# Performance work log

Hardware: AMD Instinct MI355X
Metric: run time of the kernel (lower is better)

Reference implementation:

```python
import jax, jax.numpy as jnp
import numpy as np

S, L = 4096, 12
VOCAB, CHARS, TAGS = 100000, 128, 64
CE, CH, WE, H = 64, 128, 256, 512


def setup_inputs() -> dict:
    key = jax.random.key(0)
    ks = jax.random.split(key, 16)
    n = lambda k, shp, s=0.05: (jax.random.normal(k, shp, jnp.float32) * s)
    return {
        "w_seq": jax.random.randint(ks[0], (S,), 0, VOCAB),
        "c_seq": jax.random.randint(ks[1], (S, L), 0, CHARS),
        "char_emb": n(ks[2], (CHARS, CE), 1.0),
        "word_emb": n(ks[3], (VOCAB, WE), 1.0),
        "c_hx0": jnp.zeros((CH,), jnp.float32),
        "c_cx0": jnp.zeros((CH,), jnp.float32),
        "hx0": jnp.zeros((H,), jnp.float32),
        "cx0": jnp.zeros((H,), jnp.float32),
        "Wih1": n(ks[4], (4 * CH, CE)),
        "Whh1": n(ks[5], (4 * CH, CH)),
        "bih1": n(ks[6], (4 * CH,)),
        "bhh1": n(ks[7], (4 * CH,)),
        "Wih2": n(ks[8], (4 * H, WE + CH)),
        "Whh2": n(ks[9], (4 * H, H)),
        "bih2": n(ks[10], (4 * H,)),
        "bhh2": n(ks[11], (4 * H,)),
        "W_out": n(ks[12], (TAGS, H)),
        "b_out": n(ks[13], (TAGS,)),
    }


def _lstm_step(x, h, c, Wih, Whh, b):
    # PyTorch gate order: i, f, g, o
    g = x @ Wih.T + h @ Whh.T + b
    i, f, gg, o = jnp.split(g, 4, axis=-1)
    c = jax.nn.sigmoid(f) * c + jax.nn.sigmoid(i) * jnp.tanh(gg)
    h = jax.nn.sigmoid(o) * jnp.tanh(c)
    return h, c


def reference(w_seq, c_seq, char_emb, word_emb, c_hx0, c_cx0, hx0, cx0,
              Wih1, Whh1, bih1, bhh1, Wih2, Whh2, bih2, bhh2, W_out, b_out):
    nwords = w_seq.shape[0]
    # --- batched per-word char LSTM (all words run as one batch) ---
    xs = jnp.transpose(char_emb[c_seq], (1, 0, 2))  # [L, S, CE]
    b1 = bih1 + bhh1
    h0 = jnp.broadcast_to(c_hx0, (nwords, c_hx0.shape[0]))
    c0 = jnp.broadcast_to(c_cx0, (nwords, c_cx0.shape[0]))

    def step1(carry, x):
        h, c = _lstm_step(x, carry[0], carry[1], Wih1, Whh1, b1)
        return (h, c), None

    (char_rep, _), _ = jax.lax.scan(step1, (h0, c0), xs)  # [S, CH]

    # --- word-level LSTM over the sentence ---
    wv = word_emb[w_seq]                                  # [S, WE]
    seq = jnp.concatenate([char_rep, wv], axis=1)         # [S, CH+WE]
    b2 = bih2 + bhh2

    def step2(carry, x):
        h, c = _lstm_step(x, carry[0], carry[1], Wih2, Whh2, b2)
        return (h, c), h

    _, outs = jax.lax.scan(step2, (hx0, cx0), seq)        # [S, H]

    tag_space = outs @ W_out.T + b_out                    # [S, TAGS]
    return jax.nn.log_softmax(tag_space, axis=1)
```

## Files before the change

### kernel.cpp

```cpp
#include <hip/hip_runtime.h>
#include <math.h>

#define S_LEN 4096
#define L_CH  12
#define CE    64
#define CHD   128
#define WE    256
#define HD    512
#define TAGS  64
#define GW    (4*HD)
#define XDIM  (CHD+WE)
#define NBLK  128

#define WS_GX    0
#define WS_CREP  (WS_GX   + (size_t)S_LEN*GW)
#define WS_HEXT  (WS_CREP + (size_t)S_LEN*CHD)

typedef float v4f __attribute__((ext_vector_type(4)));

static __device__ __forceinline__ float sigf(float x) {
    return 1.0f / (1.0f + __expf(-x));
}
static __device__ __forceinline__ float tanhfast(float x) {
    return 1.0f - 2.0f / (__expf(2.0f * x) + 1.0f);
}
static __device__ __forceinline__ float dot4(v4f a, v4f b) {
    return a.x*b.x + a.y*b.y + a.z*b.z + a.w*b.w;
}
template <int CTRL, int RMASK>
static __device__ __forceinline__ float dpp_add(float a) {
    int t = __builtin_amdgcn_update_dpp(0, __float_as_int(a), CTRL, RMASK, 0xf, true);
    return a + __int_as_float(t);
}
static __device__ __forceinline__ float rdlane(float v, int l) {
    return __int_as_float(__builtin_amdgcn_readlane(__float_as_int(v), l));
}

__global__ __launch_bounds__(256) void k_init(const float* __restrict__ hx0,
                                              float* __restrict__ hext) {
    size_t i = ((size_t)blockIdx.x * 256 + threadIdx.x) * 4;
    if (i >= (size_t)(S_LEN + 1) * HD) return;
    v4f v;
    if (i < HD) {
        v.x = hx0[i+0] + 2.0f; v.y = hx0[i+1] + 2.0f;
        v.z = hx0[i+2] + 2.0f; v.w = hx0[i+3] + 2.0f;
    } else {
        v.x = 0.f; v.y = 0.f; v.z = 0.f; v.w = 0.f;
    }
    float* p = hext + i;
    asm volatile("global_store_dwordx4 %0, %1, off sc0 sc1"
                 :: "v"(p), "v"(v) : "memory");
}

__global__ __launch_bounds__(256) void k_char_lstm(
    const int* __restrict__ c_seq, const float* __restrict__ char_emb,
    const float* __restrict__ c_hx0, const float* __restrict__ c_cx0,
    const float* __restrict__ Wih1, const float* __restrict__ Whh1,
    const float* __restrict__ bih1, const float* __restrict__ bhh1,
    float* __restrict__ char_rep)
{
    __shared__ float xs[16][CE + 4];
    __shared__ float hs[16][CHD + 4];
    __shared__ float cs[16][CHD + 4];
    __shared__ float gs[16][4*CHD + 4];
    const int tid = threadIdx.x;
    const int w0  = blockIdx.x * 16;

    for (int u = tid; u < 16*CHD; u += 256) {
        int w = u >> 7, k = u & (CHD-1);
        hs[w][k] = c_hx0[k];
        cs[w][k] = c_cx0[k];
    }
    __syncthreads();

    const int wg = tid & 3;
    const int rg = tid >> 2;
    const int uw = tid >> 4;
    const int uj = (tid & 15) * 8;

    for (int t = 0; t < L_CH; ++t) {
        {
            int w = tid >> 4, k4 = (tid & 15) * 4;
            int ci = c_seq[(w0 + w) * L_CH + t];
            float4 v = *(const float4*)(char_emb + (size_t)ci * CE + k4);
            *(float4*)&xs[w][k4] = v;
        }
        __syncthreads();

        float acc[8][4];
        #pragma unroll
        for (int i = 0; i < 8; ++i)
            #pragma unroll
            for (int j = 0; j < 4; ++j) acc[i][j] = 0.0f;

        for (int kc = 0; kc < CE/4; ++kc) {
            int k = kc * 4;
            float4 xv[4];
            #pragma unroll
            for (int j = 0; j < 4; ++j) xv[j] = *(const float4*)&xs[wg*4 + j][k];
            #pragma unroll
            for (int i = 0; i < 8; ++i) {
                int r = rg*8 + i;
                float4 wv = *(const float4*)(Wih1 + (size_t)r*CE + k);
                #pragma unroll
                for (int j = 0; j < 4; ++j)
                    acc[i][j] += wv.x*xv[j].x + wv.y*xv[j].y + wv.z*xv[j].z + wv.w*xv[j].w;
            }
        }
        for (int kc = 0; kc < CHD/4; ++kc) {
            int k = kc * 4;
            float4 hv[4];
            #pragma unroll
            for (int j = 0; j < 4; ++j) hv[j] = *(const float4*)&hs[wg*4 + j][k];
            #pragma unroll
            for (int i = 0; i < 8; ++i) {
                int r = rg*8 + i;
                float4 wv = *(const float4*)(Whh1 + (size_t)r*CHD + k);
                #pragma unroll
                for (int j = 0; j < 4; ++j)
                    acc[i][j] += wv.x*hv[j].x + wv.y*hv[j].y + wv.z*hv[j].z + wv.w*hv[j].w;
            }
        }
        #pragma unroll
        for (int i = 0; i < 8; ++i) {
            int r = rg*8 + i;
            float b = bih1[r] + bhh1[r];
            #pragma unroll
            for (int j = 0; j < 4; ++j) gs[wg*4 + j][r] = acc[i][j] + b;
        }
        __syncthreads();

        #pragma unroll
        for (int i = 0; i < 8; ++i) {
            int j = uj + i;
            float gi = gs[uw][j];
            float gf = gs[uw][CHD + j];
            float gg = gs[uw][2*CHD + j];
            float go = gs[uw][3*CHD + j];
            float c = sigf(gf)*cs[uw][j] + sigf(gi)*tanhfast(gg);
            cs[uw][j] = c;
            hs[uw][j] = sigf(go)*tanhfast(c);
        }
        __syncthreads();
    }
    #pragma unroll
    for (int i4 = 0; i4 < 2; ++i4) {
        float4 v;
        v.x = hs[uw][uj + i4*4 + 0]; v.y = hs[uw][uj + i4*4 + 1];
        v.z = hs[uw][uj + i4*4 + 2]; v.w = hs[uw][uj + i4*4 + 3];
        *(float4*)(char_rep + (size_t)(w0 + uw)*CHD + uj + i4*4) = v;
    }
}

__global__ __launch_bounds__(256) void k_gx(
    const int* __restrict__ w_seq, const float* __restrict__ word_emb,
    const float* __restrict__ char_rep,
    const float* __restrict__ Wih2, const float* __restrict__ bih2,
    const float* __restrict__ bhh2, float* __restrict__ Gx)
{
    __shared__ float xs[16][XDIM + 4];
    const int tid = threadIdx.x;
    const int w0  = blockIdx.x * 16;
    const int slice = blockIdx.y;

    {
        int w = tid >> 4, seg = tid & 15;
        int wsq = w_seq[w0 + w];
        #pragma unroll
        for (int i4 = 0; i4 < 6; ++i4) {
            int k = seg*24 + i4*4;
            float4 v;
            if (k < CHD) v = *(const float4*)(char_rep + (size_t)(w0+w)*CHD + k);
            else         v = *(const float4*)(word_emb + (size_t)wsq*WE + (k - CHD));
            *(float4*)&xs[w][k] = v;
        }
    }
    __syncthreads();

    const int wg = tid & 3, rg = tid >> 2;
    float acc[8][4];
    #pragma unroll
    for (int i = 0; i < 8; ++i)
        #pragma unroll
        for (int j = 0; j < 4; ++j) acc[i][j] = 0.0f;

    for (int kc = 0; kc < XDIM/4; ++kc) {
        int k = kc * 4;
        float4 xv[4];
        #pragma unroll
        for (int j = 0; j < 4; ++j) xv[j] = *(const float4*)&xs[wg*4 + j][k];
        #pragma unroll
        for (int i = 0; i < 8; ++i) {
            int r = slice*512 + rg*8 + i;
            float4 wv = *(const float4*)(Wih2 + (size_t)r*XDIM + k);
            #pragma unroll
            for (int j = 0; j < 4; ++j)
                acc[i][j] += wv.x*xv[j].x + wv.y*xv[j].y + wv.z*xv[j].z + wv.w*xv[j].w;
        }
    }
    #pragma unroll
    for (int i = 0; i < 8; ++i) {
        int r = slice*512 + rg*8 + i;
        float b = bih2[r] + bhh2[r];
        #pragma unroll
        for (int j = 0; j < 4; ++j)
            Gx[(size_t)(w0 + wg*4 + j)*GW + r] = acc[i][j] + b;
    }
}

__global__ __launch_bounds__(256, 1) void k_word_lstm(
    const float* __restrict__ Gx, const float* __restrict__ Whh2,
    const float* __restrict__ cx0, float* __restrict__ hext)
{
    const int tid  = threadIdx.x;
    const int w    = tid >> 6;
    const int lane = tid & 63;
    const int jo   = blockIdx.x * 4 + w;
    const int g2   = lane >> 5;
    const int qe   = g2 * 2, qo = qe + 1;
    const int kk   = (lane & 31) * 16;

    v4f we0, we1, we2, we3, wo0, wo1, wo2, wo3;
    {
        const float* wre = Whh2 + (size_t)(qe*HD + jo)*HD + kk;
        const float* wro = Whh2 + (size_t)(qo*HD + jo)*HD + kk;
        asm volatile(
            "global_load_dwordx4 %0, %8, off\n\t"
            "global_load_dwordx4 %1, %8, off offset:16\n\t"
            "global_load_dwordx4 %2, %8, off offset:32\n\t"
            "global_load_dwordx4 %3, %8, off offset:48\n\t"
            "global_load_dwordx4 %4, %9, off\n\t"
            "global_load_dwordx4 %5, %9, off offset:16\n\t"
            "global_load_dwordx4 %6, %9, off offset:32\n\t"
            "global_load_dwordx4 %7, %9, off offset:48\n\t"
            "s_waitcnt vmcnt(0)"
            : "=&v"(we0), "=&v"(we1), "=&v"(we2), "=&v"(we3),
              "=&v"(wo0), "=&v"(wo1), "=&v"(wo2), "=&v"(wo3)
            : "v"(wre), "v"(wro));
    }
    const float wsum_e = 2.0f * (we0.x+we0.y+we0.z+we0.w + we1.x+we1.y+we1.z+we1.w
                               + we2.x+we2.y+we2.z+we2.w + we3.x+we3.y+we3.z+we3.w);
    const float wsum_o = 2.0f * (wo0.x+wo0.y+wo0.z+wo0.w + wo1.x+wo1.y+wo1.z+wo1.w
                               + wo2.x+wo2.y+wo2.z+wo2.w + wo3.x+wo3.y+wo3.z+wo3.w);
    float creg = cx0[jo];

    for (int t = 0; t < S_LEN; ++t) {
        const float* gp = Gx + (size_t)t*GW + jo;
        float gx0 = gp[0], gx1 = gp[HD], gx2 = gp[2*HD], gx3 = gp[3*HD];

        const float* hsrc = hext + (size_t)t*HD + kk;
        v4f r0, r1, r2, r3;
        for (;;) {
            asm volatile(
                "global_load_dwordx4 %0, %4, off sc0 sc1\n\t"
                "global_load_dwordx4 %1, %4, off offset:16 sc0 sc1\n\t"
                "global_load_dwordx4 %2, %4, off offset:32 sc0 sc1\n\t"
                "global_load_dwordx4 %3, %4, off offset:48 sc0 sc1\n\t"
                "s_waitcnt vmcnt(0)"
                : "=&v"(r0), "=&v"(r1), "=&v"(r2), "=&v"(r3)
                : "v"(hsrc)
                : "memory");
            float mn = fminf(fminf(fminf(r0.x, r0.y), fminf(r0.z, r0.w)),
                             fminf(fminf(r1.x, r1.y), fminf(r1.z, r1.w)));
            mn = fminf(mn, fminf(fminf(fminf(r2.x, r2.y), fminf(r2.z, r2.w)),
                                 fminf(fminf(r3.x, r3.y), fminf(r3.z, r3.w))));
            if (__all(mn > 0.5f)) break;
        }

        float ae = dot4(we0, r0) + dot4(we1, r1) + dot4(we2, r2) + dot4(we3, r3) - wsum_e;
        float ao = dot4(wo0, r0) + dot4(wo1, r1) + dot4(wo2, r2) + dot4(wo3, r3) - wsum_o;

        ae = dpp_add<0x111, 0xf>(ae); ao = dpp_add<0x111, 0xf>(ao);
        ae = dpp_add<0x112, 0xf>(ae); ao = dpp_add<0x112, 0xf>(ao);
        ae = dpp_add<0x114, 0xf>(ae); ao = dpp_add<0x114, 0xf>(ao);
        ae = dpp_add<0x118, 0xf>(ae); ao = dpp_add<0x118, 0xf>(ao);
        ae = dpp_add<0x142, 0xa>(ae); ao = dpp_add<0x142, 0xa>(ao);

        float si = rdlane(ae, 31), sf = rdlane(ao, 31);
        float sg = rdlane(ae, 63), so = rdlane(ao, 63);

        float g0 = gx0 + si, g1 = gx1 + sf, g2v = gx2 + sg, g3 = gx3 + so;
        float c  = sigf(g1)*creg + sigf(g0)*tanhfast(g2v);
        creg = c;
        float hn = sigf(g3)*tanhfast(c) + 2.0f;
        if (lane == 0) {
            float* dst = hext + (size_t)(t+1)*HD + jo;
            asm volatile("global_store_dword %0, %1, off sc0 sc1"
                         :: "v"(dst), "v"(hn) : "memory");
        }
    }
}

__global__ __launch_bounds__(256) void k_out(
    const float* __restrict__ outs_b, const float* __restrict__ W_out,
    const float* __restrict__ b_out, float* __restrict__ out)
{
    __shared__ float hh[16][HD + 4];
    __shared__ float ts[16][TAGS + 4];
    __shared__ float lse[16];
    const int tid = threadIdx.x;
    const int w0  = blockIdx.x * 16;

    {
        int w = tid >> 4, k0 = (tid & 15) * 32;
        #pragma unroll
        for (int i4 = 0; i4 < 8; ++i4) {
            float4 v = *(const float4*)(outs_b + (size_t)(w0+w)*HD + k0 + i4*4);
            int k = k0 + i4*4;
            hh[w][k+0] = v.x - 2.0f; hh[w][k+1] = v.y - 2.0f;
            hh[w][k+2] = v.z - 2.0f; hh[w][k+3] = v.w - 2.0f;
        }
    }
    __syncthreads();

    const int tag = tid & 63;
    const int wg  = tid >> 6;
    float a0 = 0.f, a1 = 0.f, a2 = 0.f, a3 = 0.f;
    for (int kc = 0; kc < HD/4; ++kc) {
        int k = kc * 4;
        float4 wv = *(const float4*)(W_out + (size_t)tag*HD + k);
        float4 x0 = *(const float4*)&hh[wg*4+0][k];
        float4 x1 = *(const float4*)&hh[wg*4+1][k];
        float4 x2 = *(const float4*)&hh[wg*4+2][k];
        float4 x3 = *(const float4*)&hh[wg*4+3][k];
        a0 += wv.x*x0.x + wv.y*x0.y + wv.z*x0.z + wv.w*x0.w;
        a1 += wv.x*x1.x + wv.y*x1.y + wv.z*x1.z + wv.w*x1.w;
        a2 += wv.x*x2.x + wv.y*x2.y + wv.z*x2.z + wv.w*x2.w;
        a3 += wv.x*x3.x + wv.y*x3.y + wv.z*x3.z + wv.w*x3.w;
    }
    float bo = b_out[tag];
    ts[wg*4+0][tag] = a0 + bo;
    ts[wg*4+1][tag] = a1 + bo;
    ts[wg*4+2][tag] = a2 + bo;
    ts[wg*4+3][tag] = a3 + bo;
    __syncthreads();

    if (tid < 16) {
        float m = -1e30f;
        for (int q = 0; q < TAGS; ++q) m = fmaxf(m, ts[tid][q]);
        float ssum = 0.0f;
        for (int q = 0; q < TAGS; ++q) ssum += __expf(ts[tid][q] - m);
        lse[tid] = m + __logf(ssum);
    }
    __syncthreads();

    #pragma unroll
    for (int jjj = 0; jjj < 4; ++jjj)
        out[(size_t)(w0 + wg*4 + jjj)*TAGS + tag] = ts[wg*4+jjj][tag] - lse[wg*4+jjj];
}

extern "C" void kernel_launch(void* const* d_in, const int* in_sizes, int n_in,
                              void* d_out, int out_size, void* d_ws, size_t ws_size,
                              hipStream_t stream) {
    (void)in_sizes; (void)n_in; (void)out_size; (void)ws_size;
    const int*   w_seq    = (const int*)  d_in[0];
    const int*   c_seq    = (const int*)  d_in[1];
    const float* char_emb = (const float*)d_in[2];
    const float* word_emb = (const float*)d_in[3];
    const float* c_hx0    = (const float*)d_in[4];
    const float* c_cx0    = (const float*)d_in[5];
    const float* hx0      = (const float*)d_in[6];
    const float* cx0      = (const float*)d_in[7];
    const float* Wih1     = (const float*)d_in[8];
    const float* Whh1     = (const float*)d_in[9];
    const float* bih1     = (const float*)d_in[10];
    const float* bhh1     = (const float*)d_in[11];
    const float* Wih2     = (const float*)d_in[12];
    const float* Whh2     = (const float*)d_in[13];
    const float* bih2     = (const float*)d_in[14];
    const float* bhh2     = (const float*)d_in[15];
    const float* W_out    = (const float*)d_in[16];
    const float* b_out    = (const float*)d_in[17];

    float* ws   = (float*)d_ws;
    float* Gx   = ws + WS_GX;
    float* crep = ws + WS_CREP;
    float* hext = ws + WS_HEXT;

    int init_blocks = (int)(((size_t)(S_LEN + 1) * HD / 4 + 255) / 256);
    hipLaunchKernelGGL(k_init, dim3(init_blocks), dim3(256), 0, stream, hx0, hext);
    hipLaunchKernelGGL(k_char_lstm, dim3(256), dim3(256), 0, stream,
                       c_seq, char_emb, c_hx0, c_cx0, Wih1, Whh1, bih1, bhh1, crep);
    hipLaunchKernelGGL(k_gx, dim3(256, 4), dim3(256), 0, stream,
                       w_seq, word_emb, crep, Wih2, bih2, bhh2, Gx);
    hipLaunchKernelGGL(k_word_lstm, dim3(NBLK), dim3(256), 0, stream,
                       Gx, Whh2, cx0, hext);
    hipLaunchKernelGGL(k_out, dim3(256), dim3(256), 0, stream,
                       hext + HD, W_out, b_out, (float*)d_out);
}
```

Baseline: 10.70 ms.

## Give each wave four hidden units in the word LSTM and use fewer blocks

The recurrent word-LSTM kernel now has each wavefront compute four output units instead of one, so the grid shrinks from 128 blocks to 32. Each wave keeps four times as many Whh2 rows in registers and reads Gx with float4 loads. Each block gathers its 16 new h values in shared memory and publishes them with 16 stores. The aim is fewer blocks polling the shared h buffer each step, at the cost of four times more compute per wave, higher register pressure and an extra __syncthreads per timestep.

```diff
diff --git a/kernel.cpp b/kernel.cpp
--- a/kernel.cpp
+++ b/kernel.cpp
@@ -10,7 +10,7 @@
 #define TAGS  64
 #define GW    (4*HD)
 #define XDIM  (CHD+WE)
-#define NBLK  128
+#define NBLK  32
 
 #define WS_GX    0
 #define WS_CREP  (WS_GX   + (size_t)S_LEN*GW)
@@ -212,18 +212,22 @@
     const float* __restrict__ Gx, const float* __restrict__ Whh2,
     const float* __restrict__ cx0, float* __restrict__ hext)
 {
+    __shared__ __align__(16) float hsh[2][16];
     const int tid  = threadIdx.x;
     const int w    = tid >> 6;
     const int lane = tid & 63;
-    const int jo   = blockIdx.x * 4 + w;
+    const int jb   = blockIdx.x * 16;
+    const int jo4  = jb + w * 4;
     const int g2   = lane >> 5;
     const int qe   = g2 * 2, qo = qe + 1;
     const int kk   = (lane & 31) * 16;
 
-    v4f we0, we1, we2, we3, wo0, wo1, wo2, wo3;
-    {
-        const float* wre = Whh2 + (size_t)(qe*HD + jo)*HD + kk;
-        const float* wro = Whh2 + (size_t)(qo*HD + jo)*HD + kk;
+    v4f we_[4][4], wo_[4][4];
+    float wse[4], wso[4];
+    #pragma unroll
+    for (int o = 0; o < 4; ++o) {
+        const float* pe = Whh2 + (size_t)(qe*HD + jo4 + o)*HD + kk;
+        const float* po = Whh2 + (size_t)(qo*HD + jo4 + o)*HD + kk;
         asm volatile(
             "global_load_dwordx4 %0, %8, off\n\t"
             "global_load_dwordx4 %1, %8, off offset:16\n\t"
@@ -234,19 +238,36 @@
             "global_load_dwordx4 %6, %9, off offset:32\n\t"
             "global_load_dwordx4 %7, %9, off offset:48\n\t"
             "s_waitcnt vmcnt(0)"
-            : "=&v"(we0), "=&v"(we1), "=&v"(we2), "=&v"(we3),
-              "=&v"(wo0), "=&v"(wo1), "=&v"(wo2), "=&v"(wo3)
-            : "v"(wre), "v"(wro));
-    }
-    const float wsum_e = 2.0f * (we0.x+we0.y+we0.z+we0.w + we1.x+we1.y+we1.z+we1.w
-                               + we2.x+we2.y+we2.z+we2.w + we3.x+we3.y+we3.z+we3.w);
-    const float wsum_o = 2.0f * (wo0.x+wo0.y+wo0.z+wo0.w + wo1.x+wo1.y+wo1.z+wo1.w
-                               + wo2.x+wo2.y+wo2.z+wo2.w + wo3.x+wo3.y+wo3.z+wo3.w);
-    float creg = cx0[jo];
+            : "=&v"(we_[o][0]), "=&v"(we_[o][1]), "=&v"(we_[o][2]), "=&v"(we_[o][3]),
+              "=&v"(wo_[o][0]), "=&v"(wo_[o][1]), "=&v"(wo_[o][2]), "=&v"(wo_[o][3])
+            : "v"(pe), "v"(po));
+        wse[o] = 2.0f * (we_[o][0].x+we_[o][0].y+we_[o][0].z+we_[o][0].w
+                       + we_[o][1].x+we_[o][1].y+we_[o][1].z+we_[o][1].w
+                       + we_[o][2].x+we_[o][2].y+we_[o][2].z+we_[o][2].w
+                       + we_[o][3].x+we_[o][3].y+we_[o][3].z+we_[o][3].w);
+        wso[o] = 2.0f * (wo_[o][0].x+wo_[o][0].y+wo_[o][0].z+wo_[o][0].w
+                       + wo_[o][1].x+wo_[o][1].y+wo_[o][1].z+wo_[o][1].w
+                       + wo_[o][2].x+wo_[o][2].y+wo_[o][2].z+wo_[o][2].w
+                       + wo_[o][3].x+wo_[o][3].y+wo_[o][3].z+wo_[o][3].w);
+    }
+
+    float creg[4];
+    #pragma unroll
+    for (int o = 0; o < 4; ++o) creg[o] = cx0[jo4 + o];
 
     for (int t = 0; t < S_LEN; ++t) {
-        const float* gp = Gx + (size_t)t*GW + jo;
-        float gx0 = gp[0], gx1 = gp[HD], gx2 = gp[2*HD], gx3 = gp[3*HD];
+        const float* gp = Gx + (size_t)t*GW + jo4;
+        float gxa[4][4];
+        {
+            float4 v0 = *(const float4*)(gp);
+            float4 v1 = *(const float4*)(gp + HD);
+            float4 v2 = *(const float4*)(gp + 2*HD);
+            float4 v3 = *(const float4*)(gp + 3*HD);
+            gxa[0][0]=v0.x; gxa[0][1]=v0.y; gxa[0][2]=v0.z; gxa[0][3]=v0.w;
+            gxa[1][0]=v1.x; gxa[1][1]=v1.y; gxa[1][2]=v1.z; gxa[1][3]=v1.w;
+            gxa[2][0]=v2.x; gxa[2][1]=v2.y; gxa[2][2]=v2.z; gxa[2][3]=v2.w;
+            gxa[3][0]=v3.x; gxa[3][1]=v3.y; gxa[3][2]=v3.z; gxa[3][3]=v3.w;
+        }
 
         const float* hsrc = hext + (size_t)t*HD + kk;
         v4f r0, r1, r2, r3;
@@ -267,26 +288,48 @@
             if (__all(mn > 0.5f)) break;
         }
 
-        float ae = dot4(we0, r0) + dot4(we1, r1) + dot4(we2, r2) + dot4(we3, r3) - wsum_e;
-        float ao = dot4(wo0, r0) + dot4(wo1, r1) + dot4(wo2, r2) + dot4(wo3, r3) - wsum_o;
-
-        ae = dpp_add<0x111, 0xf>(ae); ao = dpp_add<0x111, 0xf>(ao);
-        ae = dpp_add<0x112, 0xf>(ae); ao = dpp_add<0x112, 0xf>(ao);
-        ae = dpp_add<0x114, 0xf>(ae); ao = dpp_add<0x114, 0xf>(ao);
-        ae = dpp_add<0x118, 0xf>(ae); ao = dpp_add<0x118, 0xf>(ao);
-        ae = dpp_add<0x142, 0xa>(ae); ao = dpp_add<0x142, 0xa>(ao);
-
-        float si = rdlane(ae, 31), sf = rdlane(ao, 31);
-        float sg = rdlane(ae, 63), so = rdlane(ao, 63);
-
-        float g0 = gx0 + si, g1 = gx1 + sf, g2v = gx2 + sg, g3 = gx3 + so;
-        float c  = sigf(g1)*creg + sigf(g0)*tanhfast(g2v);
-        creg = c;
-        float hn = sigf(g3)*tanhfast(c) + 2.0f;
+        float ae[4], ao[4];
+        #pragma unroll
+        for (int o = 0; o < 4; ++o) {
+            ae[o] = dot4(we_[o][0], r0) + dot4(we_[o][1], r1)
+                  + dot4(we_[o][2], r2) + dot4(we_[o][3], r3) - wse[o];
+            ao[o] = dot4(wo_[o][0], r0) + dot4(wo_[o][1], r1)
+                  + dot4(wo_[o][2], r2) + dot4(wo_[o][3], r3) - wso[o];
+        }
+
+        #pragma unroll
+        for (int o = 0; o < 4; ++o) {
+            ae[o] = dpp_add<0x111, 0xf>(ae[o]); ao[o] = dpp_add<0x111, 0xf>(ao[o]);
+            ae[o] = dpp_add<0x112, 0xf>(ae[o]); ao[o] = dpp_add<0x112, 0xf>(ao[o]);
+            ae[o] = dpp_add<0x114, 0xf>(ae[o]); ao[o] = dpp_add<0x114, 0xf>(ao[o]);
+            ae[o] = dpp_add<0x118, 0xf>(ae[o]); ao[o] = dpp_add<0x118, 0xf>(ao[o]);
+            ae[o] = dpp_add<0x142, 0xa>(ae[o]); ao[o] = dpp_add<0x142, 0xa>(ao[o]);
+        }
+
+        float hn[4];
+        #pragma unroll
+        for (int o = 0; o < 4; ++o) {
+            float si = rdlane(ae[o], 31), sf = rdlane(ao[o], 31);
+            float sg = rdlane(ae[o], 63), so = rdlane(ao[o], 63);
+            float g0 = gxa[0][o] + si;
+            float g1 = gxa[1][o] + sf;
+            float g2v = gxa[2][o] + sg;
+            float g3 = gxa[3][o] + so;
+            float c  = sigf(g1)*creg[o] + sigf(g0)*tanhfast(g2v);
+            creg[o] = c;
+            hn[o] = sigf(g3)*tanhfast(c) + 2.0f;
+        }
+
         if (lane == 0) {
-            float* dst = hext + (size_t)(t+1)*HD + jo;
+            float4 hv; hv.x = hn[0]; hv.y = hn[1]; hv.z = hn[2]; hv.w = hn[3];
+            *(float4*)&hsh[t & 1][w*4] = hv;
+        }
+        __syncthreads();
+        if (tid < 16) {
+            float v = hsh[t & 1][tid];
+            float* dst = hext + (size_t)(t+1)*HD + jb + tid;
             asm volatile("global_store_dword %0, %1, off sc0 sc1"
-                         :: "v"(dst), "v"(hn) : "memory");
+                         :: "v"(dst), "v"(v) : "memory");
         }
     }
 }
```

Measured after the change: 10.99 ms. +2.8%, slower.
